# Kernel optimization log

Hardware: AMD Instinct MI355X
Metric: run time of the kernel (lower is better)

The kernel has to match this reference:

```python
import jax, jax.numpy as jnp
import numpy as np

VOCAB = 50257
EMBED = 256
UNITS = 1024   # dec_units == attention units == GRU units
ENC_D = 1024   # encoder feature dim
B = 64
T_ENC = 128


def setup_inputs() -> dict:
    key = jax.random.key(0)
    ks = jax.random.split(key, 16)
    s = lambda k, *sh: jax.random.normal(k, sh, dtype=jnp.float32) * 0.02
    gru_in = ENC_D + EMBED  # concat(context, embedding)
    return {
        "x": jax.random.randint(ks[0], (B, 1), 0, VOCAB),
        "hidden": jax.random.normal(ks[1], (B, UNITS), dtype=jnp.float32),
        "enc_output": jax.random.normal(ks[2], (B, T_ENC, ENC_D), dtype=jnp.float32),
        "emb": s(ks[3], VOCAB, EMBED),
        "W1": s(ks[4], UNITS, UNITS), "b1": jnp.zeros((UNITS,), jnp.float32),
        "W2": s(ks[5], ENC_D, UNITS), "b2": jnp.zeros((UNITS,), jnp.float32),
        "V": s(ks[6], UNITS, 1), "bV": jnp.zeros((1,), jnp.float32),
        "gru_kernel": s(ks[7], gru_in, 3 * UNITS),
        "gru_rkernel": s(ks[8], UNITS, 3 * UNITS),
        "gru_bias": jnp.zeros((2, 3 * UNITS), jnp.float32),  # reset_after=True: [input_bias, recurrent_bias]
        "fcW": s(ks[9], UNITS, VOCAB), "fcb": jnp.zeros((VOCAB,), jnp.float32),
    }


def reference(x, hidden, enc_output, emb, W1, b1, W2, b2, V, bV,
              gru_kernel, gru_rkernel, gru_bias, fcW, fcb):
    # --- Bahdanau attention ---
    q = hidden[:, None, :] @ W1 + b1                    # [B,1,U]
    k = enc_output @ W2 + b2                            # [B,T,U]
    score = jnp.tanh(q + k) @ V + bV                    # [B,T,1]
    attw = jax.nn.softmax(score, axis=1)                # [B,T,1]
    context = jnp.sum(attw * enc_output, axis=1)        # [B,ENC_D]

    # --- embed token and concat (single time step) ---
    e = emb[x[:, 0]]                                    # [B,EMBED]
    xin = jnp.concatenate([context, e], axis=-1)        # [B,ENC_D+EMBED]

    # --- single GRU step (keras default reset_after=True), initial state zeros
    # (original code calls self.gru(x) without initial_state) ---
    h0 = jnp.zeros((xin.shape[0], UNITS), xin.dtype)
    xz, xr, xh = jnp.split(xin @ gru_kernel + gru_bias[0], 3, axis=-1)
    rz, rr, rh = jnp.split(h0 @ gru_rkernel + gru_bias[1], 3, axis=-1)
    z = jax.nn.sigmoid(xz + rz)
    r = jax.nn.sigmoid(xr + rr)
    hh = jnp.tanh(xh + r * rh)
    h = z * h0 + (1.0 - z) * hh                          # [B,U]

    logits = h @ fcW + fcb                               # [B,VOCAB]
    return logits, h, attw
```

## Files before the change

### kernel.cpp

```cpp
#include <hip/hip_runtime.h>
#include <hip/hip_bf16.h>

#define UNITS 1024
#define EMBED 256
#define TENC  128
#define BATCH 64
#define VOCAB 50257
#define GRU_IN 1280
#define MROWS 8192
#define NCB   8
#define NSPLIT 8

typedef __bf16 bf16x8 __attribute__((ext_vector_type(8)));
typedef __bf16 bf16x2 __attribute__((ext_vector_type(2)));
typedef float  f32x4  __attribute__((ext_vector_type(4)));
typedef float  f32x4u __attribute__((ext_vector_type(4), aligned(4)));

__global__ __launch_bounds__(256) void gemm_splitk(
    const float* __restrict__ A, const float* __restrict__ B,
    float* __restrict__ Cpart, int M, int N, int K, int Kc)
{
  const int col0  = blockIdx.y * 64;
  const int kbase = blockIdx.z * Kc;
  const int tid  = threadIdx.x;
  const int lane = tid & 63;
  const int wid  = tid >> 6;
  const int wm   = (wid >> 1) * 32;
  const int wn   = (wid & 1) * 32;

  __shared__ __bf16 As[2][4][64][8];
  __shared__ __bf16 Bs[2][4][64][8];

  f32x4 acc[2][2] = {};

  const int ar  = tid >> 2;
  const int akc = (tid & 3) * 8;
  const int bkk = tid >> 4;
  const int bn  = (tid & 15) * 4;

  f32x4 pa0[2], pa1[2], pb0[2], pb1[2];

  auto LOAD = [&](int k0, int s) {
    const float* ap = A + (size_t)ar * K + k0 + akc;
    pa0[s] = *reinterpret_cast<const f32x4*>(ap);
    pa1[s] = *reinterpret_cast<const f32x4*>(ap + 4);
    const float* bp0 = B + (size_t)(k0 + bkk) * N + col0 + bn;
    pb0[s] = *reinterpret_cast<const f32x4*>(bp0);
    pb1[s] = *reinterpret_cast<const f32x4*>(bp0 + (size_t)16 * N);
  };
  auto STAGE = [&](int s, int bb) {
    bf16x8 v;
#pragma unroll
    for (int j = 0; j < 4; ++j) { v[j] = (__bf16)pa0[s][j]; v[4 + j] = (__bf16)pa1[s][j]; }
    *reinterpret_cast<bf16x8*>(&As[bb][tid & 3][ar][0]) = v;
#pragma unroll
    for (int j = 0; j < 4; ++j) {
      Bs[bb][bkk >> 3][bn + j][bkk & 7]               = (__bf16)pb0[s][j];
      Bs[bb][(bkk + 16) >> 3][bn + j][(bkk + 16) & 7] = (__bf16)pb1[s][j];
    }
  };
  auto COMPUTE = [&](int bb) {
    bf16x8 af[2], bfr[2];
#pragma unroll
    for (int f = 0; f < 2; ++f) {
      af[f]  = *reinterpret_cast<const bf16x8*>(&As[bb][lane >> 4][wm + f * 16 + (lane & 15)][0]);
      bfr[f] = *reinterpret_cast<const bf16x8*>(&Bs[bb][lane >> 4][wn + f * 16 + (lane & 15)][0]);
    }
#pragma unroll
    for (int fm = 0; fm < 2; ++fm)
#pragma unroll
      for (int fn = 0; fn < 2; ++fn)
        acc[fm][fn] = __builtin_amdgcn_mfma_f32_16x16x32_bf16(af[fm], bfr[fn], acc[fm][fn], 0, 0, 0);
  };

  const int nt = Kc >> 5;
  LOAD(kbase, 0);
  LOAD(kbase + 32, 1);
  STAGE(0, 0);
  __syncthreads();
  for (int t = 0; t < nt; t += 2) {
    if (t + 2 < nt) LOAD(kbase + ((t + 2) << 5), 0);
    COMPUTE(0);
    if (t + 1 < nt) STAGE(1, 1);
    __syncthreads();
    if (t + 1 < nt) {
      if (t + 3 < nt) LOAD(kbase + ((t + 3) << 5), 1);
      COMPUTE(1);
      if (t + 2 < nt) STAGE(0, 0);
      __syncthreads();
    }
  }

  float* Cz = Cpart + (size_t)blockIdx.z * M * N;
#pragma unroll
  for (int fm = 0; fm < 2; ++fm) {
    const int rbase = wm + fm * 16 + (lane >> 4) * 4;
#pragma unroll
    for (int fn = 0; fn < 2; ++fn) {
      const int gc = col0 + wn + fn * 16 + (lane & 15);
#pragma unroll
      for (int r = 0; r < 4; ++r)
        Cz[(size_t)(rbase + r) * N + gc] = acc[fm][fn][r];
    }
  }
}

__global__ __launch_bounds__(256) void gemm_fc(
    const float* __restrict__ A, const float* __restrict__ B,
    const float* __restrict__ bias, float* __restrict__ C, int N)
{
  const int col0 = blockIdx.x * 64;
  const int tid  = threadIdx.x;
  const int lane = tid & 63;
  const int wid  = tid >> 6;
  const int wm   = (wid >> 1) * 32;
  const int wn   = (wid & 1) * 32;

  __shared__ __bf16 As[2][4][64][8];
  __shared__ __bf16 Bs[2][4][64][8];

  f32x4 acc[2][2] = {};

  const int ar  = tid >> 2;
  const int akc = (tid & 3) * 8;
  const int bkk = tid >> 4;
  const int bn  = (tid & 15) * 4;
  const int gn  = col0 + bn;
  const bool okb = (gn + 3 < N);

  f32x4 pa0[2], pa1[2], pb0[2], pb1[2];

  auto LOAD = [&](int k0, int s) {
    const float* ap = A + (size_t)ar * UNITS + k0 + akc;
    pa0[s] = *reinterpret_cast<const f32x4*>(ap);
    pa1[s] = *reinterpret_cast<const f32x4*>(ap + 4);
    const float* bp0 = B + (size_t)(k0 + bkk) * N + gn;
    const float* bp1 = bp0 + (size_t)16 * N;
    if (okb) {
      pb0[s] = *reinterpret_cast<const f32x4u*>(bp0);
      pb1[s] = *reinterpret_cast<const f32x4u*>(bp1);
    } else {
      f32x4 t0 = {0,0,0,0}, t1 = {0,0,0,0};
#pragma unroll
      for (int j = 0; j < 4; ++j)
        if (gn + j < N) { t0[j] = bp0[j]; t1[j] = bp1[j]; }
      pb0[s] = t0; pb1[s] = t1;
    }
  };
  auto STAGE = [&](int s, int bb) {
    bf16x8 v;
#pragma unroll
    for (int j = 0; j < 4; ++j) { v[j] = (__bf16)pa0[s][j]; v[4 + j] = (__bf16)pa1[s][j]; }
    *reinterpret_cast<bf16x8*>(&As[bb][tid & 3][ar][0]) = v;
#pragma unroll
    for (int j = 0; j < 4; ++j) {
      Bs[bb][bkk >> 3][bn + j][bkk & 7]               = (__bf16)pb0[s][j];
      Bs[bb][(bkk + 16) >> 3][bn + j][(bkk + 16) & 7] = (__bf16)pb1[s][j];
    }
  };
  auto COMPUTE = [&](int bb) {
    bf16x8 af[2], bfr[2];
#pragma unroll
    for (int f = 0; f < 2; ++f) {
      af[f]  = *reinterpret_cast<const bf16x8*>(&As[bb][lane >> 4][wm + f * 16 + (lane & 15)][0]);
      bfr[f] = *reinterpret_cast<const bf16x8*>(&Bs[bb][lane >> 4][wn + f * 16 + (lane & 15)][0]);
    }
#pragma unroll
    for (int fm = 0; fm < 2; ++fm)
#pragma unroll
      for (int fn = 0; fn < 2; ++fn)
        acc[fm][fn] = __builtin_amdgcn_mfma_f32_16x16x32_bf16(af[fm], bfr[fn], acc[fm][fn], 0, 0, 0);
  };

  LOAD(0, 0);
  LOAD(32, 1);
  STAGE(0, 0);
  __syncthreads();
#pragma unroll 1
  for (int t = 0; t < 32; t += 2) {
    if (t + 2 < 32) LOAD((t + 2) << 5, 0);
    COMPUTE(0);
    STAGE(1, 1);
    __syncthreads();
    if (t + 3 < 32) LOAD((t + 3) << 5, 1);
    COMPUTE(1);
    if (t + 2 < 32) STAGE(0, 0);
    __syncthreads();
  }

#pragma unroll
  for (int fm = 0; fm < 2; ++fm) {
    const int rbase = wm + fm * 16 + (lane >> 4) * 4;
#pragma unroll
    for (int fn = 0; fn < 2; ++fn) {
      const int gc = col0 + wn + fn * 16 + (lane & 15);
      if (gc >= N) continue;
      const float bv = bias[gc];
#pragma unroll
      for (int r = 0; r < 4; ++r)
        __builtin_nontemporal_store(acc[fm][fn][r] + bv, &C[(size_t)(rbase + r) * N + gc]);
    }
  }
}

__global__ __launch_bounds__(256) void gemm_k_score(
    const float* __restrict__ enc, const float* __restrict__ W2,
    const float* __restrict__ b1, const float* __restrict__ b2,
    const float* __restrict__ qpart, const float* __restrict__ Vw,
    float* __restrict__ partial)
{
  const int b    = blockIdx.x;
  const int row0 = b * TENC;
  const int col0 = blockIdx.y * 128;
  const int tid  = threadIdx.x;
  const int lane = tid & 63;
  const int wid  = tid >> 6;
  const int wm   = (wid >> 1) * 64;
  const int wn   = (wid & 1) * 64;

  __shared__ __bf16 As[4][128][8];
  __shared__ __bf16 Bs[4][128][8];
  __shared__ float  sred[2][128];

  f32x4 acc[4][4] = {};

  const int ar  = tid >> 1;
  const int ak  = (tid & 1) * 16;
  const int kkp = (tid >> 4) * 2;
  const int c0  = (tid & 15) * 8;

  f32x4 pa[4], pb[4];

  auto LOAD = [&](int k0) {
    const float* ap = enc + (size_t)(row0 + ar) * UNITS + k0 + ak;
    pa[0] = *reinterpret_cast<const f32x4*>(ap);
    pa[1] = *reinterpret_cast<const f32x4*>(ap + 4);
    pa[2] = *reinterpret_cast<const f32x4*>(ap + 8);
    pa[3] = *reinterpret_cast<const f32x4*>(ap + 12);
    const float* bp0 = W2 + (size_t)(k0 + kkp) * UNITS + col0 + c0;
    pb[0] = *reinterpret_cast<const f32x4*>(bp0);
    pb[1] = *reinterpret_cast<const f32x4*>(bp0 + 4);
    pb[2] = *reinterpret_cast<const f32x4*>(bp0 + UNITS);
    pb[3] = *reinterpret_cast<const f32x4*>(bp0 + UNITS + 4);
  };

  LOAD(0);
  for (int t = 0; t < 32; ++t) {
    __syncthreads();
    {
      bf16x8 v0, v1;
#pragma unroll
      for (int j = 0; j < 4; ++j) {
        v0[j] = (__bf16)pa[0][j]; v0[4 + j] = (__bf16)pa[1][j];
        v1[j] = (__bf16)pa[2][j]; v1[4 + j] = (__bf16)pa[3][j];
      }
      *reinterpret_cast<bf16x8*>(&As[(ak >> 3) + 0][ar][0]) = v0;
      *reinterpret_cast<bf16x8*>(&As[(ak >> 3) + 1][ar][0]) = v1;
      const int bch = kkp >> 3, bk = kkp & 7;
#pragma unroll
      for (int j = 0; j < 8; ++j) {
        const float lo = (j < 4) ? pb[0][j] : pb[1][j - 4];
        const float hi = (j < 4) ? pb[2][j] : pb[3][j - 4];
        bf16x2 pr = { (__bf16)lo, (__bf16)hi };
        *reinterpret_cast<bf16x2*>(&Bs[bch][c0 + j][bk]) = pr;
      }
    }
    __syncthreads();
    if (t + 1 < 32) LOAD((t + 1) << 5);

    bf16x8 af[4], bfr[4];
#pragma unroll
    for (int f = 0; f < 4; ++f) {
      af[f]  = *reinterpret_cast<const bf16x8*>(&As[lane >> 4][wm + f * 16 + (lane & 15)][0]);
      bfr[f] = *reinterpret_cast<const bf16x8*>(&Bs[lane >> 4][wn + f * 16 + (lane & 15)][0]);
    }
#pragma unroll
    for (int fm = 0; fm < 4; ++fm)
#pragma unroll
      for (int fn = 0; fn < 4; ++fn)
        acc[fm][fn] = __builtin_amdgcn_mfma_f32_16x16x32_bf16(af[fm], bfr[fn], acc[fm][fn], 0, 0, 0);
  }

  float rowsum[4][4] = {};
#pragma unroll
  for (int fn = 0; fn < 4; ++fn) {
    const int gc = col0 + wn + fn * 16 + (lane & 15);
    float qv = b1[gc] + b2[gc];
#pragma unroll
    for (int s = 0; s < NSPLIT; ++s)
      qv += qpart[(size_t)s * BATCH * UNITS + (size_t)b * UNITS + gc];
    const float vv = Vw[gc];
#pragma unroll
    for (int fm = 0; fm < 4; ++fm)
#pragma unroll
      for (int r = 0; r < 4; ++r)
        rowsum[fm][r] += tanhf(qv + acc[fm][fn][r]) * vv;
  }
#pragma unroll
  for (int off = 8; off; off >>= 1)
#pragma unroll
    for (int fm = 0; fm < 4; ++fm)
#pragma unroll
      for (int r = 0; r < 4; ++r)
        rowsum[fm][r] += __shfl_xor(rowsum[fm][r], off);
  if ((lane & 15) == 0) {
#pragma unroll
    for (int fm = 0; fm < 4; ++fm)
#pragma unroll
      for (int r = 0; r < 4; ++r)
        sred[wid & 1][wm + fm * 16 + (lane >> 4) * 4 + r] = rowsum[fm][r];
  }
  __syncthreads();
  if (tid < TENC)
    partial[(size_t)blockIdx.y * MROWS + row0 + tid] = sred[0][tid] + sred[1][tid];
}

__global__ __launch_bounds__(256) void ctx_kernel(
    const float* __restrict__ enc, const float* __restrict__ partial,
    const float* __restrict__ bV, const float* __restrict__ emb,
    const int* __restrict__ x, float* __restrict__ attw,
    float* __restrict__ xin)
{
  const int b   = blockIdx.x;
  const int tid = threadIdx.x;
  __shared__ float scs[TENC];
  __shared__ float red[4];

  if (tid < TENC) {
    float s = bV[0];
#pragma unroll
    for (int cb = 0; cb < NCB; ++cb) s += partial[(size_t)cb * MROWS + b * TENC + tid];
    float m = s;
#pragma unroll
    for (int off = 32; off; off >>= 1) m = fmaxf(m, __shfl_xor(m, off));
    if ((tid & 63) == 0) red[tid >> 6] = m;
    scs[tid] = s;
  }
  __syncthreads();
  const float mm = fmaxf(red[0], red[1]);
  if (tid < TENC) {
    const float e = expf(scs[tid] - mm);
    scs[tid] = e;
    float su = e;
#pragma unroll
    for (int off = 32; off; off >>= 1) su += __shfl_xor(su, off);
    if ((tid & 63) == 0) red[2 + (tid >> 6)] = su;
  }
  __syncthreads();
  const float inv = 1.f / (red[2] + red[3]);
  if (tid < TENC) scs[tid] *= inv;
  __syncthreads();

  if (blockIdx.y == 0 && tid < TENC) attw[(size_t)b * TENC + tid] = scs[tid];

  const int n = blockIdx.y * 256 + tid;
  const float* ep = enc + (size_t)b * TENC * UNITS + n;
  float c = 0.f;
#pragma unroll 8
  for (int t = 0; t < TENC; ++t) c += scs[t] * ep[(size_t)t * UNITS];
  xin[(size_t)b * GRU_IN + n] = c;
  if (blockIdx.y == 0)
    xin[(size_t)b * GRU_IN + UNITS + tid] = emb[(size_t)x[b] * EMBED + tid];
}

__global__ __launch_bounds__(256) void gru_pw(
    const float* __restrict__ gpart, const float* __restrict__ gb0,
    const float* __restrict__ gb1, float* __restrict__ h)
{
  const int i = blockIdx.x * 256 + threadIdx.x;
  const int b = i >> 10, n = i & 1023;
  float xz = gb0[n], xr = gb0[1024 + n], xh = gb0[2048 + n];
#pragma unroll
  for (int s = 0; s < NSPLIT; ++s) {
    const float* g = gpart + (size_t)s * BATCH * 3072 + (size_t)b * 3072;
    xz += g[n]; xr += g[1024 + n]; xh += g[2048 + n];
  }
  const float rz = gb1[n], rr = gb1[1024 + n], rh = gb1[2048 + n];
  const float z = 1.f / (1.f + expf(-(xz + rz)));
  const float r = 1.f / (1.f + expf(-(xr + rr)));
  const float hh = tanhf(xh + r * rh);
  h[i] = (1.f - z) * hh;
}

extern "C" void kernel_launch(void* const* d_in, const int* in_sizes, int n_in,
                              void* d_out, int out_size, void* d_ws, size_t ws_size,
                              hipStream_t stream)
{
  (void)in_sizes; (void)n_in; (void)out_size; (void)ws_size;
  const int*   x      = (const int*)  d_in[0];
  const float* hidden = (const float*)d_in[1];
  const float* enc    = (const float*)d_in[2];
  const float* emb    = (const float*)d_in[3];
  const float* W1     = (const float*)d_in[4];
  const float* b1     = (const float*)d_in[5];
  const float* W2     = (const float*)d_in[6];
  const float* b2     = (const float*)d_in[7];
  const float* Vw     = (const float*)d_in[8];
  const float* bV     = (const float*)d_in[9];
  const float* gk     = (const float*)d_in[10];
  const float* gb     = (const float*)d_in[12];
  const float* fcW    = (const float*)d_in[13];
  const float* fcb    = (const float*)d_in[14];

  float* ws      = (float*)d_ws;
  float* qpart   = ws;
  float* partial = qpart + 524288;
  float* xin     = partial + 65536;
  float* gpart   = xin + 81920;

  float* out    = (float*)d_out;
  float* logits = out;
  float* hout   = out + (size_t)BATCH * VOCAB;
  float* attw   = hout + BATCH * UNITS;

  hipLaunchKernelGGL(gemm_splitk, dim3(1, 16, NSPLIT), dim3(256), 0, stream,
                     hidden, W1, qpart, 64, 1024, 1024, 128);
  hipLaunchKernelGGL(gemm_k_score, dim3(64, NCB), dim3(256), 0, stream,
                     enc, W2, b1, b2, qpart, Vw, partial);
  hipLaunchKernelGGL(ctx_kernel, dim3(64, 4), dim3(256), 0, stream,
                     enc, partial, bV, emb, x, attw, xin);
  hipLaunchKernelGGL(gemm_splitk, dim3(1, 48, NSPLIT), dim3(256), 0, stream,
                     xin, gk, gpart, 64, 3072, 1280, 160);
  hipLaunchKernelGGL(gru_pw, dim3(256), dim3(256), 0, stream,
                     gpart, gb, gb + 3072, hout);
  hipLaunchKernelGGL(gemm_fc, dim3((VOCAB + 63) / 64), dim3(256), 0, stream,
                     hout, fcW, fcb, logits, VOCAB);
}
```

Baseline: 153.2 us.

## Pre-convert enc and W2 to bf16 and stream tiles via global_load_lds

Adds a conversion kernel that casts enc_output to bf16 and writes a transposed bf16 copy of W2 into workspace. The score GEMM then loads 16-byte bf16 chunks straight into LDS with global_load_lds and doubles the K-tile to 64. This removes the per-tile fp32 loads, in-register conversion and scattered bf16x2 LDS stores. The cost is an extra full pass over the 32MB enc tensor and W2 every call, plus the loss of the register prefetch that overlapped the next tile's loads with MFMA work.

```diff
diff --git a/kernel.cpp b/kernel.cpp
--- a/kernel.cpp
+++ b/kernel.cpp
@@ -12,9 +12,52 @@
 #define NSPLIT 8
 
 typedef __bf16 bf16x8 __attribute__((ext_vector_type(8)));
-typedef __bf16 bf16x2 __attribute__((ext_vector_type(2)));
 typedef float  f32x4  __attribute__((ext_vector_type(4)));
 typedef float  f32x4u __attribute__((ext_vector_type(4), aligned(4)));
+
+__device__ __forceinline__ void gload_lds16(const void* gsrc, void* ldst) {
+  __builtin_amdgcn_global_load_lds(
+      (const __attribute__((address_space(1))) void*)gsrc,
+      (__attribute__((address_space(3))) void*)ldst,
+      16, 0, 0);
+}
+
+__global__ __launch_bounds__(256) void convert_kernel(
+    const float* __restrict__ enc, const float* __restrict__ W2,
+    __bf16* __restrict__ encb, __bf16* __restrict__ w2t)
+{
+  __shared__ __bf16 tl[64][72];
+  const int bid = blockIdx.x;
+  const int tid = threadIdx.x;
+  if (bid < 4096) {
+    const size_t base = ((size_t)bid * 256 + tid) * 8;
+    const f32x4 v0 = *reinterpret_cast<const f32x4*>(enc + base);
+    const f32x4 v1 = *reinterpret_cast<const f32x4*>(enc + base + 4);
+    bf16x8 o;
+#pragma unroll
+    for (int j = 0; j < 4; ++j) { o[j] = (__bf16)v0[j]; o[4 + j] = (__bf16)v1[j]; }
+    *reinterpret_cast<bf16x8*>(encb + base) = o;
+  } else {
+    const int ti  = bid - 4096;
+    const int kt0 = (ti >> 4) * 64, nt0 = (ti & 15) * 64;
+    const int r = tid >> 2, q = (tid & 3) * 16;
+    const float* wp = W2 + (size_t)(kt0 + r) * UNITS + nt0 + q;
+#pragma unroll
+    for (int v = 0; v < 4; ++v) {
+      const f32x4 a = *reinterpret_cast<const f32x4*>(wp + v * 4);
+#pragma unroll
+      for (int j = 0; j < 4; ++j) tl[r][q + v * 4 + j] = (__bf16)a[j];
+    }
+    __syncthreads();
+    const int n = tid >> 2, kq = (tid & 3) * 16;
+    bf16x8 o0, o1;
+#pragma unroll
+    for (int j = 0; j < 8; ++j) { o0[j] = tl[kq + j][n]; o1[j] = tl[kq + 8 + j][n]; }
+    __bf16* op = w2t + (size_t)(nt0 + n) * UNITS + kt0 + kq;
+    *reinterpret_cast<bf16x8*>(op)     = o0;
+    *reinterpret_cast<bf16x8*>(op + 8) = o1;
+  }
+}
 
 __global__ __launch_bounds__(256) void gemm_splitk(
     const float* __restrict__ A, const float* __restrict__ B,
@@ -203,8 +246,8 @@
   }
 }
 
-__global__ __launch_bounds__(256) void gemm_k_score(
-    const float* __restrict__ enc, const float* __restrict__ W2,
+__global__ __launch_bounds__(256) void k_score_mfma(
+    const __bf16* __restrict__ encb, const __bf16* __restrict__ w2t,
     const float* __restrict__ b1, const float* __restrict__ b2,
     const float* __restrict__ qpart, const float* __restrict__ Vw,
     float* __restrict__ partial)
@@ -218,67 +261,40 @@
   const int wm   = (wid >> 1) * 64;
   const int wn   = (wid & 1) * 64;
 
-  __shared__ __bf16 As[4][128][8];
-  __shared__ __bf16 Bs[4][128][8];
+  __shared__ __bf16 As[8][128][8];
+  __shared__ __bf16 Bs[8][128][8];
   __shared__ float  sred[2][128];
 
   f32x4 acc[4][4] = {};
 
-  const int ar  = tid >> 1;
-  const int ak  = (tid & 1) * 16;
-  const int kkp = (tid >> 4) * 2;
-  const int c0  = (tid & 15) * 8;
-
-  f32x4 pa[4], pb[4];
-
-  auto LOAD = [&](int k0) {
-    const float* ap = enc + (size_t)(row0 + ar) * UNITS + k0 + ak;
-    pa[0] = *reinterpret_cast<const f32x4*>(ap);
-    pa[1] = *reinterpret_cast<const f32x4*>(ap + 4);
-    pa[2] = *reinterpret_cast<const f32x4*>(ap + 8);
-    pa[3] = *reinterpret_cast<const f32x4*>(ap + 12);
-    const float* bp0 = W2 + (size_t)(k0 + kkp) * UNITS + col0 + c0;
-    pb[0] = *reinterpret_cast<const f32x4*>(bp0);
-    pb[1] = *reinterpret_cast<const f32x4*>(bp0 + 4);
-    pb[2] = *reinterpret_cast<const f32x4*>(bp0 + UNITS);
-    pb[3] = *reinterpret_cast<const f32x4*>(bp0 + UNITS + 4);
-  };
-
-  LOAD(0);
-  for (int t = 0; t < 32; ++t) {
-    __syncthreads();
-    {
-      bf16x8 v0, v1;
-#pragma unroll
-      for (int j = 0; j < 4; ++j) {
-        v0[j] = (__bf16)pa[0][j]; v0[4 + j] = (__bf16)pa[1][j];
-        v1[j] = (__bf16)pa[2][j]; v1[4 + j] = (__bf16)pa[3][j];
+  for (int t = 0; t < 16; ++t) {
+    const int k0 = t * 64;
+#pragma unroll
+    for (int j = 0; j < 4; ++j) {
+      const int i  = wid * 4 + j;
+      const int c  = i >> 1, rh = (i & 1) * 64;
+      const __bf16* ga = encb + (size_t)(row0 + rh + lane) * UNITS + k0 + c * 8;
+      gload_lds16(ga, &As[c][rh][0]);
+      const __bf16* gb = w2t + (size_t)(col0 + rh + lane) * UNITS + k0 + c * 8;
+      gload_lds16(gb, &Bs[c][rh][0]);
+    }
+    __syncthreads();
+
+#pragma unroll
+    for (int s = 0; s < 2; ++s) {
+      bf16x8 af[4], bfr[4];
+#pragma unroll
+      for (int f = 0; f < 4; ++f) {
+        af[f]  = *reinterpret_cast<const bf16x8*>(&As[s * 4 + (lane >> 4)][wm + f * 16 + (lane & 15)][0]);
+        bfr[f] = *reinterpret_cast<const bf16x8*>(&Bs[s * 4 + (lane >> 4)][wn + f * 16 + (lane & 15)][0]);
       }
-      *reinterpret_cast<bf16x8*>(&As[(ak >> 3) + 0][ar][0]) = v0;
-      *reinterpret_cast<bf16x8*>(&As[(ak >> 3) + 1][ar][0]) = v1;
-      const int bch = kkp >> 3, bk = kkp & 7;
-#pragma unroll
-      for (int j = 0; j < 8; ++j) {
-        const float lo = (j < 4) ? pb[0][j] : pb[1][j - 4];
-        const float hi = (j < 4) ? pb[2][j] : pb[3][j - 4];
-        bf16x2 pr = { (__bf16)lo, (__bf16)hi };
-        *reinterpret_cast<bf16x2*>(&Bs[bch][c0 + j][bk]) = pr;
-      }
-    }
-    __syncthreads();
-    if (t + 1 < 32) LOAD((t + 1) << 5);
-
-    bf16x8 af[4], bfr[4];
-#pragma unroll
-    for (int f = 0; f < 4; ++f) {
-      af[f]  = *reinterpret_cast<const bf16x8*>(&As[lane >> 4][wm + f * 16 + (lane & 15)][0]);
-      bfr[f] = *reinterpret_cast<const bf16x8*>(&Bs[lane >> 4][wn + f * 16 + (lane & 15)][0]);
-    }
-#pragma unroll
-    for (int fm = 0; fm < 4; ++fm)
-#pragma unroll
-      for (int fn = 0; fn < 4; ++fn)
-        acc[fm][fn] = __builtin_amdgcn_mfma_f32_16x16x32_bf16(af[fm], bfr[fn], acc[fm][fn], 0, 0, 0);
+#pragma unroll
+      for (int fm = 0; fm < 4; ++fm)
+#pragma unroll
+        for (int fn = 0; fn < 4; ++fn)
+          acc[fm][fn] = __builtin_amdgcn_mfma_f32_16x16x32_bf16(af[fm], bfr[fn], acc[fm][fn], 0, 0, 0);
+    }
+    __syncthreads();
   }
 
   float rowsum[4][4] = {};
@@ -407,16 +423,20 @@
   float* partial = qpart + 524288;
   float* xin     = partial + 65536;
   float* gpart   = xin + 81920;
+  __bf16* encb   = (__bf16*)(gpart + 1572864);
+  __bf16* w2t    = encb + (size_t)MROWS * UNITS;
 
   float* out    = (float*)d_out;
   float* logits = out;
   float* hout   = out + (size_t)BATCH * VOCAB;
   float* attw   = hout + BATCH * UNITS;
 
+  hipLaunchKernelGGL(convert_kernel, dim3(4096 + 256), dim3(256), 0, stream,
+                     enc, W2, encb, w2t);
   hipLaunchKernelGGL(gemm_splitk, dim3(1, 16, NSPLIT), dim3(256), 0, stream,
                      hidden, W1, qpart, 64, 1024, 1024, 128);
-  hipLaunchKernelGGL(gemm_k_score, dim3(64, NCB), dim3(256), 0, stream,
-                     enc, W2, b1, b2, qpart, Vw, partial);
+  hipLaunchKernelGGL(k_score_mfma, dim3(64, NCB), dim3(256), 0, stream,
+                     encb, w2t, b1, b2, qpart, Vw, partial);
   hipLaunchKernelGGL(ctx_kernel, dim3(64, 4), dim3(256), 0, stream,
                      enc, partial, bV, emb, x, attw, xin);
   hipLaunchKernelGGL(gemm_splitk, dim3(1, 48, NSPLIT), dim3(256), 0, stream,
```

Result: faster. 146.2 us (-4.5%).
